# Performance work log

Measured on AMD Instinct MI355X. Metric: run time of the kernel, lower is better.

The kernel has to match this reference:

```python
import jax, jax.numpy as jnp
import numpy as np

N, E = 50000, 800000
IN_CH, HID, OUT = 128, 64, 64
H1, H2 = 4, 1
NEG_SLOPE = 0.2  # PyG GATConv default


def _glorot(key, shape):
    fan_in, fan_out = shape[0], shape[-1]
    lim = (6.0 / (fan_in + fan_out)) ** 0.5
    return jax.random.uniform(key, shape, jnp.float32, -lim, lim)


def setup_inputs() -> dict:
    key = jax.random.key(0)
    ks = jax.random.split(key, 12)
    x = jax.random.normal(ks[0], (N, IN_CH), jnp.float32)
    edge_index = jax.random.randint(ks[1], (2, E), 0, N, jnp.int64)
    # layer 1: in_ch -> hid, 4 heads, concat
    W1 = _glorot(ks[2], (IN_CH, H1 * HID))
    a_src1 = _glorot(ks[3], (H1, HID))
    a_dst1 = _glorot(ks[4], (H1, HID))
    b1 = jnp.zeros((H1 * HID,), jnp.float32)
    # layer 2: hid*4 -> out, 1 head, mean (concat=False)
    W2 = _glorot(ks[5], (H1 * HID, H2 * OUT))
    a_src2 = _glorot(ks[6], (H2, OUT))
    a_dst2 = _glorot(ks[7], (H2, OUT))
    b2 = jnp.zeros((OUT,), jnp.float32)
    return {"x": x, "edge_index": edge_index, "W1": W1, "a_src1": a_src1,
            "a_dst1": a_dst1, "b1": b1, "W2": W2, "a_src2": a_src2,
            "a_dst2": a_dst2, "b2": b2}


def gat_layer(x, src, dst, W, a_src, a_dst, b, concat):
    n = x.shape[0]
    Hh, Fh = a_src.shape
    h = (x @ W).reshape(n, Hh, Fh)                      # [N,H,F]
    al_src = jnp.sum(h * a_src[None], axis=-1)          # [N,H]
    al_dst = jnp.sum(h * a_dst[None], axis=-1)          # [N,H]
    logits = jax.nn.leaky_relu(al_src[src] + al_dst[dst], NEG_SLOPE)  # [E,H]
    # numerically stable segment softmax over destination nodes
    mx = jax.ops.segment_max(logits, dst, num_segments=n)
    mx = jnp.where(jnp.isfinite(mx), mx, 0.0)
    e = jnp.exp(logits - mx[dst])                       # [E,H]
    denom = jax.ops.segment_sum(e, dst, num_segments=n)  # [N,H]
    alpha = e / jnp.maximum(denom[dst], 1e-16)          # [E,H]
    msg = h[src] * alpha[:, :, None]                    # [E,H,F]
    out = jax.ops.segment_sum(msg, dst, num_segments=n)  # [N,H,F]
    out = out.reshape(n, Hh * Fh) if concat else out.mean(axis=1)
    return out + b


def reference(x, edge_index, W1, a_src1, a_dst1, b1, W2, a_src2, a_dst2, b2):
    n = x.shape[0]
    # PyG GATConv adds self-loops by default
    loops = jnp.arange(n, dtype=edge_index.dtype)
    src = jnp.concatenate([edge_index[0], loops])
    dst = jnp.concatenate([edge_index[1], loops])
    h = gat_layer(x, src, dst, W1, a_src1, a_dst1, b1, concat=True)
    h = jax.nn.elu(h)
    # dropout is identity in eval mode
    out = gat_layer(h, src, dst, W2, a_src2, a_dst2, b2, concat=False)
    return out
```

## Files before the change

kernel.cpp:

```cpp
#include <hip/hip_runtime.h>
#include <math.h>

#define NEG_SLOPE 0.2f
#define SLOTS 64

typedef unsigned short ushort_t;
typedef _Float16 f16x8 __attribute__((ext_vector_type(8)));
typedef _Float16 h2v  __attribute__((ext_vector_type(2)));
typedef float f32x4v __attribute__((ext_vector_type(4)));

__device__ __forceinline__ float leaky(float x) { return x > 0.f ? x : NEG_SLOPE * x; }

__device__ __forceinline__ ushort_t f2h(float f) {
    union { _Float16 h; ushort_t u; } v; v.h = (_Float16)f; return v.u;
}
__device__ __forceinline__ unsigned packh(float a, float b) {
    union { h2v h; unsigned u; } c; c.h[0] = (_Float16)a; c.h[1] = (_Float16)b; return c.u;
}

__global__ __launch_bounds__(256) void k_prep0(const float* __restrict__ W1, const float* __restrict__ W2,
                                               const float* __restrict__ as1, const float* __restrict__ ad1,
                                               const float* __restrict__ as2, const float* __restrict__ ad2,
                                               ushort_t* __restrict__ W1t, ushort_t* __restrict__ W2t,
                                               float* __restrict__ va1s, float* __restrict__ va1d,
                                               float* __restrict__ va2s, float* __restrict__ va2d) {
    int b = blockIdx.x, t = threadIdx.x;
    if (b < 256) {
        if (t < 128) W1t[b * 128 + t] = f2h(W1[t * 256 + b]);
    } else if (b < 320) {
        int n = b - 256;
        W2t[n * 256 + t] = f2h(W2[t * 64 + n]);
    } else if (b == 320) {
        for (int idx = t; idx < 1024; idx += 256) {
            int k = idx >> 3, h = (idx >> 1) & 3, sd = idx & 1;
            const float* a = sd ? ad1 : as1;
            float acc = 0.f;
            for (int f = 0; f < 64; ++f) acc += W1[k * 256 + h * 64 + f] * a[h * 64 + f];
            (sd ? va1d : va1s)[k * 4 + h] = acc;
        }
    } else {
        for (int idx = t; idx < 512; idx += 256) {
            int k = idx >> 1, sd = idx & 1;
            const float* a = sd ? ad2 : as2;
            float acc = 0.f;
            for (int f = 0; f < 64; ++f) acc += W2[k * 64 + f] * a[f];
            (sd ? va2d : va2s)[k] = acc;
        }
    }
}

__global__ __launch_bounds__(256) void k_prep1(const int* __restrict__ ei, int E, int EB,
                                               int* __restrict__ cnt, ushort_t* __restrict__ csr,
                                               const float* __restrict__ x,
                                               const float* __restrict__ va1s, const float* __restrict__ va1d,
                                               ushort_t* __restrict__ xh,
                                               float4* __restrict__ alS, float4* __restrict__ alD,
                                               int N, int NB) {
    int b = blockIdx.x, t = threadIdx.x;
    if (b < EB) {
        int i = b * 256 + t;
        if (i < E) {
            int s = ei[i];
            int d = ei[E + i];
            int p = atomicAdd(&cnt[d], 1);
            if (p < SLOTS - 1) csr[d * SLOTS + 1 + p] = (ushort_t)s;
        }
        return;
    }
    b -= EB;
    if (b < NB) {
        int n = b * 256 + t;
        if (n < N) csr[n * SLOTS] = (ushort_t)n;
        return;
    }
    b -= NB;
    int r = b * 16 + (t >> 4);
    int idx = t & 15;
    if (r >= N) return;
    const float* xr = x + (size_t)r * 128 + idx * 8;
    float4 f0 = *(const float4*)xr;
    float4 f1 = *(const float4*)(xr + 4);
    uint4 pv;
    pv.x = packh(f0.x, f0.y); pv.y = packh(f0.z, f0.w);
    pv.z = packh(f1.x, f1.y); pv.w = packh(f1.z, f1.w);
    *(uint4*)&xh[(size_t)r * 128 + idx * 8] = pv;
    float xs[8] = {f0.x, f0.y, f0.z, f0.w, f1.x, f1.y, f1.z, f1.w};
    float s0 = 0, s1 = 0, s2 = 0, s3 = 0, d0 = 0, d1 = 0, d2 = 0, d3 = 0;
    #pragma unroll
    for (int j = 0; j < 8; ++j) {
        int k = idx * 8 + j;
        float4 vs = *(const float4*)&va1s[k * 4];
        float4 vd = *(const float4*)&va1d[k * 4];
        s0 += xs[j] * vs.x; s1 += xs[j] * vs.y; s2 += xs[j] * vs.z; s3 += xs[j] * vs.w;
        d0 += xs[j] * vd.x; d1 += xs[j] * vd.y; d2 += xs[j] * vd.z; d3 += xs[j] * vd.w;
    }
    #pragma unroll
    for (int off = 8; off >= 1; off >>= 1) {
        s0 += __shfl_xor(s0, off, 64); s1 += __shfl_xor(s1, off, 64);
        s2 += __shfl_xor(s2, off, 64); s3 += __shfl_xor(s3, off, 64);
        d0 += __shfl_xor(d0, off, 64); d1 += __shfl_xor(d1, off, 64);
        d2 += __shfl_xor(d2, off, 64); d3 += __shfl_xor(d3, off, 64);
    }
    if (idx == 0) {
        alS[r] = make_float4(s0, s1, s2, s3);
        alD[r] = make_float4(d0, d1, d2, d3);
    }
}

#define CONS(p, a) do { \
    _Float16 ah_ = (_Float16)(a); \
    h2v a2_ = {ah_, ah_}; \
    union { uint4 u; h2v h[4]; } c_; c_.u = (p); \
    ha0 += c_.h[0] * a2_; ha1 += c_.h[1] * a2_; \
    ha2 += c_.h[2] * a2_; ha3 += c_.h[3] * a2_; } while (0)

#define FLUSH() do { \
    acc[0] += (float)ha0[0]; acc[1] += (float)ha0[1]; \
    acc[2] += (float)ha1[0]; acc[3] += (float)ha1[1]; \
    acc[4] += (float)ha2[0]; acc[5] += (float)ha2[1]; \
    acc[6] += (float)ha3[0]; acc[7] += (float)ha3[1]; \
    ha0 = (h2v)0; ha1 = (h2v)0; ha2 = (h2v)0; ha3 = (h2v)0; } while (0)

__global__ __launch_bounds__(256) void k_agg1(const int* __restrict__ cnt, const ushort_t* __restrict__ csr,
                                              const float4* __restrict__ alS4, const float4* __restrict__ alD4,
                                              const ushort_t* __restrict__ xh,
                                              ushort_t* __restrict__ aggh, int N) {
    __shared__ float s_alpha[4][SLOTS][4];
    __shared__ int   s_off[4][SLOTS];
    int w = threadIdx.x >> 6, lane = threadIdx.x & 63;
    int n = blockIdx.x * 4 + w;
    if (n >= N) return;
    int stored = cnt[n]; if (stored > SLOTS - 1) stored = SLOTS - 1;
    int deg = stored + 1;
    int s = 0;
    if (lane < deg) s = csr[(size_t)n * SLOTS + lane];
    s_off[w][lane] = (lane < deg) ? (s << 8) : 0;

    float e0 = 0.f, e1 = 0.f, e2 = 0.f, e3 = 0.f;
    if (lane < deg) {
        float4 ald = alD4[n];
        float4 as = alS4[s];
        e0 = __expf(leaky(as.x + ald.x));
        e1 = __expf(leaky(as.y + ald.y));
        e2 = __expf(leaky(as.z + ald.z));
        e3 = __expf(leaky(as.w + ald.w));
    }
    *(float4*)&s_alpha[w][lane][0] = make_float4(e0, e1, e2, e3);

    int head = lane >> 4, cid = lane & 15;
    const char* xb = (const char*)xh + cid * 16;

    float acc[8];
    #pragma unroll
    for (int i = 0; i < 8; ++i) acc[i] = 0.f;
    h2v ha0 = (h2v)0, ha1 = (h2v)0, ha2 = (h2v)0, ha3 = (h2v)0;

    int nit = (deg + 3) & ~3;

    int4 ovA = *(const int4*)&s_off[w][0];
    uint4 pA0 = *(const uint4*)(xb + ovA.x);
    uint4 pA1 = *(const uint4*)(xb + ovA.y);
    uint4 pA2 = *(const uint4*)(xb + ovA.z);
    uint4 pA3 = *(const uint4*)(xb + ovA.w);

    for (int j = 0; j < nit; j += 8) {
        uint4 pB0, pB1, pB2, pB3;
        bool hasB = (j + 4 < nit);
        if (hasB) {
            int4 ovB = *(const int4*)&s_off[w][j + 4];
            pB0 = *(const uint4*)(xb + ovB.x);
            pB1 = *(const uint4*)(xb + ovB.y);
            pB2 = *(const uint4*)(xb + ovB.z);
            pB3 = *(const uint4*)(xb + ovB.w);
        }
        {
            float a0 = s_alpha[w][j + 0][head];
            float a1 = s_alpha[w][j + 1][head];
            float a2 = s_alpha[w][j + 2][head];
            float a3 = s_alpha[w][j + 3][head];
            CONS(pA0, a0); CONS(pA1, a1); CONS(pA2, a2); CONS(pA3, a3);
        }
        if (hasB) {
            if (j + 8 < nit) {
                int4 ovA2 = *(const int4*)&s_off[w][j + 8];
                pA0 = *(const uint4*)(xb + ovA2.x);
                pA1 = *(const uint4*)(xb + ovA2.y);
                pA2 = *(const uint4*)(xb + ovA2.z);
                pA3 = *(const uint4*)(xb + ovA2.w);
            }
            float a0 = s_alpha[w][j + 4][head];
            float a1 = s_alpha[w][j + 5][head];
            float a2 = s_alpha[w][j + 6][head];
            float a3 = s_alpha[w][j + 7][head];
            CONS(pB0, a0); CONS(pB1, a1); CONS(pB2, a2); CONS(pB3, a3);
        }
        FLUSH();
    }

    float d0 = e0, d1 = e1, d2 = e2, d3 = e3;
    #pragma unroll
    for (int off = 32; off >= 1; off >>= 1) {
        d0 += __shfl_xor(d0, off, 64); d1 += __shfl_xor(d1, off, 64);
        d2 += __shfl_xor(d2, off, 64); d3 += __shfl_xor(d3, off, 64);
    }
    float dh = head == 0 ? d0 : head == 1 ? d1 : head == 2 ? d2 : d3;
    float inv = 1.f / fmaxf(dh, 1e-16f);

    uint4 u;
    u.x = packh(acc[0] * inv, acc[1] * inv);
    u.y = packh(acc[2] * inv, acc[3] * inv);
    u.z = packh(acc[4] * inv, acc[5] * inv);
    u.w = packh(acc[6] * inv, acc[7] * inv);
    *(uint4*)(aggh + (size_t)n * 512 + head * 128 + cid * 8) = u;
}
#undef CONS
#undef FLUSH

__global__ __launch_bounds__(256) void k_gemmO(const ushort_t* __restrict__ aggh, const ushort_t* __restrict__ W1t,
                                               const ushort_t* __restrict__ W2t,
                                               const float* __restrict__ b1,
                                               const float* __restrict__ va2s, const float* __restrict__ va2d,
                                               ushort_t* __restrict__ h2h,
                                               float* __restrict__ al2S, float* __restrict__ al2D, int N) {
    __shared__ ushort_t sU[4 * 64 * 136];
    __shared__ float s_al2w[4][64][2];
    int t = threadIdx.x;
    int w = t >> 6, lane = t & 63;
    int m = lane & 15, quad = lane >> 4;
    int r0 = blockIdx.x * 64;

    #pragma unroll
    for (int q = 0; q < 16; ++q) {
        int idx = t + q * 256;
        int row = idx >> 6, off = idx & 63;
        int gr = r0 + row;
        uint4 v = (gr < N) ? *(const uint4*)(aggh + (size_t)gr * 512 + off * 8)
                           : make_uint4(0, 0, 0, 0);
        int h = off >> 4, k8 = off & 15;
        *(uint4*)&sU[(size_t)(h * 64 + row) * 136 + k8 * 8] = v;
    }
    __syncthreads();

    f32x4v acc[4][4];
    #pragma unroll
    for (int r = 0; r < 4; ++r)
        #pragma unroll
        for (int cg = 0; cg < 4; ++cg) acc[r][cg] = (f32x4v){0.f, 0.f, 0.f, 0.f};
    #pragma unroll
    for (int ks = 0; ks < 4; ++ks) {
        f16x8 af[4];
        #pragma unroll
        for (int r = 0; r < 4; ++r)
            af[r] = *(f16x8*)&sU[(size_t)(w * 64 + r * 16 + m) * 136 + ks * 32 + quad * 8];
        #pragma unroll
        for (int cg = 0; cg < 4; ++cg) {
            f16x8 bf = *(f16x8*)&W1t[(size_t)(w * 64 + cg * 16 + m) * 128 + ks * 32 + quad * 8];
            #pragma unroll
            for (int r = 0; r < 4; ++r)
                acc[r][cg] = __builtin_amdgcn_mfma_f32_16x16x32_f16(af[r], bf, acc[r][cg], 0, 0, 0);
        }
    }
    __syncthreads();

    ushort_t* sO = sU;
    float ps[4][4], pd[4][4];
    #pragma unroll
    for (int r = 0; r < 4; ++r)
        #pragma unroll
        for (int reg = 0; reg < 4; ++reg) { ps[r][reg] = 0.f; pd[r][reg] = 0.f; }
    #pragma unroll
    for (int cg = 0; cg < 4; ++cg) {
        int c = w * 64 + cg * 16 + m;
        float bias = b1[c];
        float v2s = va2s[c], v2d = va2d[c];
        #pragma unroll
        for (int r = 0; r < 4; ++r)
            #pragma unroll
            for (int reg = 0; reg < 4; ++reg) {
                int row = r * 16 + quad * 4 + reg;
                float v = acc[r][cg][reg] + bias;
                v = v > 0.f ? v : (__expf(v) - 1.f);
                sO[(size_t)row * 264 + c] = f2h(v);
                ps[r][reg] += v * v2s;
                pd[r][reg] += v * v2d;
            }
    }
    #pragma unroll
    for (int off = 1; off <= 8; off <<= 1)
        #pragma unroll
        for (int r = 0; r < 4; ++r)
            #pragma unroll
            for (int reg = 0; reg < 4; ++reg) {
                ps[r][reg] += __shfl_xor(ps[r][reg], off, 64);
                pd[r][reg] += __shfl_xor(pd[r][reg], off, 64);
            }
    if (m == 0) {
        #pragma unroll
        for (int r = 0; r < 4; ++r)
            #pragma unroll
            for (int reg = 0; reg < 4; ++reg) {
                int row = r * 16 + quad * 4 + reg;
                s_al2w[w][row][0] = ps[r][reg];
                s_al2w[w][row][1] = pd[r][reg];
            }
    }
    __syncthreads();

    if (t < 64) {
        int gr = r0 + t;
        if (gr < N) {
            float a = 0.f, b = 0.f;
            #pragma unroll
            for (int w2 = 0; w2 < 4; ++w2) { a += s_al2w[w2][t][0]; b += s_al2w[w2][t][1]; }
            al2S[gr] = a; al2D[gr] = b;
        }
    }

    f32x4v acc2[4];
    #pragma unroll
    for (int r = 0; r < 4; ++r) acc2[r] = (f32x4v){0.f, 0.f, 0.f, 0.f};
    #pragma unroll
    for (int kb = 0; kb < 2; ++kb)
        #pragma unroll
        for (int ks = 0; ks < 4; ++ks) {
            int kk = kb * 128 + ks * 32 + quad * 8;
            f16x8 bf = *(f16x8*)&W2t[(size_t)(w * 16 + m) * 256 + kk];
            #pragma unroll
            for (int r = 0; r < 4; ++r) {
                f16x8 af = *(f16x8*)&sO[(size_t)(r * 16 + m) * 264 + kk];
                acc2[r] = __builtin_amdgcn_mfma_f32_16x16x32_f16(af, bf, acc2[r], 0, 0, 0);
            }
        }
    int col = w * 16 + m;
    #pragma unroll
    for (int r = 0; r < 4; ++r) {
        int gr0 = r0 + r * 16 + quad * 4;
        #pragma unroll
        for (int reg = 0; reg < 4; ++reg) {
            int gr = gr0 + reg;
            if (gr < N) h2h[(size_t)gr * 64 + col] = f2h(acc2[r][reg]);
        }
    }
}

__global__ __launch_bounds__(256) void k_agg2(const int* __restrict__ cnt, const ushort_t* __restrict__ csr,
                                              const float* __restrict__ alS, const float* __restrict__ alD,
                                              const ushort_t* __restrict__ h2h, const float* __restrict__ b2,
                                              float* __restrict__ out, int N) {
    int lane = threadIdx.x & 63;
    int n = blockIdx.x * 4 + (threadIdx.x >> 6);
    if (n >= N) return;
    int stored = cnt[n]; if (stored > SLOTS - 1) stored = SLOTS - 1;
    int deg = stored + 1;
    const ushort_t* crow = csr + (size_t)n * SLOTS;

    int s0 = 0;
    if (lane < deg) s0 = crow[lane];

    int grp = lane >> 3, cid = lane & 7;
    int choff = cid * 16;
    const char* hbase = (const char*)h2h;

    uint4 pbuf[3];
    #pragma unroll
    for (int i = 0; i < 3; ++i) {
        int sj = __shfl(s0, i * 8 + grp, 64);
        pbuf[i] = *(const uint4*)(hbase + ((size_t)sj << 7) + choff);
    }

    float ald = alD[n];
    float e0 = 0.f;
    if (lane < deg) e0 = __expf(leaky(alS[s0] + ald));

    h2v ha0 = (h2v)0, ha1 = (h2v)0, ha2 = (h2v)0, ha3 = (h2v)0;
    #pragma unroll
    for (int i = 0; i < 3; ++i) {
        float a = __shfl(e0, i * 8 + grp, 64);
        union { uint4 u; h2v h[4]; } c; c.u = pbuf[i];
        _Float16 ah = (_Float16)a;
        h2v a2 = {ah, ah};
        ha0 += c.h[0] * a2; ha1 += c.h[1] * a2;
        ha2 += c.h[2] * a2; ha3 += c.h[3] * a2;
    }
    for (int j = 24; j < deg; j += 8) {
        int jj = j + grp;
        float a = __shfl(e0, jj, 64);
        int sj = __shfl(s0, jj, 64);
        union { uint4 u; h2v h[4]; } c;
        c.u = *(const uint4*)(hbase + ((size_t)sj << 7) + choff);
        _Float16 ah = (_Float16)a;
        h2v a2 = {ah, ah};
        ha0 += c.h[0] * a2; ha1 += c.h[1] * a2;
        ha2 += c.h[2] * a2; ha3 += c.h[3] * a2;
    }

    float den = e0;
    #pragma unroll
    for (int off = 32; off >= 1; off >>= 1) den += __shfl_xor(den, off, 64);
    float inv = 1.f / fmaxf(den, 1e-16f);

    float acc[8];
    acc[0] = (float)ha0[0]; acc[1] = (float)ha0[1];
    acc[2] = (float)ha1[0]; acc[3] = (float)ha1[1];
    acc[4] = (float)ha2[0]; acc[5] = (float)ha2[1];
    acc[6] = (float)ha3[0]; acc[7] = (float)ha3[1];
    #pragma unroll
    for (int off = 8; off <= 32; off <<= 1)
        #pragma unroll
        for (int i = 0; i < 8; ++i) acc[i] += __shfl_xor(acc[i], off, 64);

    if (grp == 0) {
        int c8 = cid * 8;
        float4 b0 = *(const float4*)&b2[c8];
        float4 b1v = *(const float4*)&b2[c8 + 4];
        float4 o0 = make_float4(acc[0]*inv + b0.x, acc[1]*inv + b0.y, acc[2]*inv + b0.z, acc[3]*inv + b0.w);
        float4 o1 = make_float4(acc[4]*inv + b1v.x, acc[5]*inv + b1v.y, acc[6]*inv + b1v.z, acc[7]*inv + b1v.w);
        *(float4*)(out + (size_t)n * 64 + c8) = o0;
        *(float4*)(out + (size_t)n * 64 + c8 + 4) = o1;
    }
}

extern "C" void kernel_launch(void* const* d_in, const int* in_sizes, int n_in,
                              void* d_out, int out_size, void* d_ws, size_t ws_size,
                              hipStream_t stream) {
    const float* x      = (const float*)d_in[0];
    const int*   ei     = (const int*)d_in[1];
    const float* W1     = (const float*)d_in[2];
    const float* a_src1 = (const float*)d_in[3];
    const float* a_dst1 = (const float*)d_in[4];
    const float* b1     = (const float*)d_in[5];
    const float* W2     = (const float*)d_in[6];
    const float* a_src2 = (const float*)d_in[7];
    const float* a_dst2 = (const float*)d_in[8];
    const float* b2     = (const float*)d_in[9];
    float* out = (float*)d_out;

    int N = in_sizes[0] / 128;
    int E = in_sizes[1] / 2;

    char* ws = (char*)d_ws;
    size_t off = 0;
    auto alloc = [&](size_t bytes) -> void* {
        void* p = ws + off;
        off = (off + bytes + 255) & ~(size_t)255;
        return p;
    };
    ushort_t* xh    = (ushort_t*)alloc((size_t)N * 128 * 2);
    ushort_t* aggh  = (ushort_t*)alloc((size_t)N * 512 * 2);
    ushort_t* h2h   = (ushort_t*)alloc((size_t)N * 64 * 2);
    ushort_t* W1t   = (ushort_t*)alloc(256 * 128 * 2);
    ushort_t* W2t   = (ushort_t*)alloc(64 * 256 * 2);
    float* va1s  = (float*)alloc(128 * 4 * 4);
    float* va1d  = (float*)alloc(128 * 4 * 4);
    float* va2s  = (float*)alloc(256 * 4);
    float* va2d  = (float*)alloc(256 * 4);
    float* alS1  = (float*)alloc((size_t)N * 4 * 4);
    float* alD1  = (float*)alloc((size_t)N * 4 * 4);
    float* alS2  = (float*)alloc((size_t)N * 4);
    float* alD2  = (float*)alloc((size_t)N * 4);
    int*   cnt   = (int*)alloc((size_t)N * 4);
    ushort_t* csr = (ushort_t*)alloc((size_t)N * SLOTS * 2);
    (void)ws_size; (void)n_in; (void)out_size;

    int EB  = (E + 255) / 256;
    int NB  = (N + 255) / 256;
    int XB  = (N + 15) / 16;
    int AB1 = (N + 3) / 4;
    int GO  = (N + 63) / 64;
    int NC4 = (N + 3) / 4;

    hipMemsetAsync(cnt, 0, (size_t)N * 4, stream);

    k_prep0<<<322, 256, 0, stream>>>(W1, W2, a_src1, a_dst1, a_src2, a_dst2,
                                     W1t, W2t, va1s, va1d, va2s, va2d);
    k_prep1<<<EB + NB + XB, 256, 0, stream>>>(ei, E, EB, cnt, csr, x, va1s, va1d,
                                              xh, (float4*)alS1, (float4*)alD1, N, NB);
    k_agg1<<<AB1, 256, 0, stream>>>(cnt, csr,
                                    (const float4*)alS1, (const float4*)alD1,
                                    xh, aggh, N);
    k_gemmO<<<GO, 256, 0, stream>>>(aggh, W1t, W2t, b1, va2s, va2d,
                                    h2h, alS2, alD2, N);
    k_agg2<<<NC4, 256, 0, stream>>>(cnt, csr, alS2, alD2, h2h, b2, out, N);
}
```

Measured before the change: 261.9 us.

## Bucket edge scatter into eight sub-CSRs then merge per node

After: 269.3 us. +2.8%, slower.

```diff
diff --git a/kernel.cpp b/kernel.cpp
--- a/kernel.cpp
+++ b/kernel.cpp
@@ -3,6 +3,7 @@
 
 #define NEG_SLOPE 0.2f
 #define SLOTS 64
+#define XSLOTS 24
 
 typedef unsigned short ushort_t;
 typedef _Float16 f16x8 __attribute__((ext_vector_type(8)));
@@ -50,30 +51,25 @@
 }
 
 __global__ __launch_bounds__(256) void k_prep1(const int* __restrict__ ei, int E, int EB,
-                                               int* __restrict__ cnt, ushort_t* __restrict__ csr,
+                                               int* __restrict__ cnt8, ushort_t* __restrict__ csr8,
                                                const float* __restrict__ x,
                                                const float* __restrict__ va1s, const float* __restrict__ va1d,
                                                ushort_t* __restrict__ xh,
                                                float4* __restrict__ alS, float4* __restrict__ alD,
-                                               int N, int NB) {
+                                               int N) {
     int b = blockIdx.x, t = threadIdx.x;
     if (b < EB) {
         int i = b * 256 + t;
         if (i < E) {
             int s = ei[i];
             int d = ei[E + i];
-            int p = atomicAdd(&cnt[d], 1);
-            if (p < SLOTS - 1) csr[d * SLOTS + 1 + p] = (ushort_t)s;
+            int bkt = b & 7;
+            int p = atomicAdd(&cnt8[bkt * N + d], 1);
+            if (p < XSLOTS) csr8[((size_t)bkt * N + d) * XSLOTS + p] = (ushort_t)s;
         }
         return;
     }
     b -= EB;
-    if (b < NB) {
-        int n = b * 256 + t;
-        if (n < N) csr[n * SLOTS] = (ushort_t)n;
-        return;
-    }
-    b -= NB;
     int r = b * 16 + (t >> 4);
     int idx = t & 15;
     if (r >= N) return;
@@ -105,6 +101,29 @@
         alS[r] = make_float4(s0, s1, s2, s3);
         alD[r] = make_float4(d0, d1, d2, d3);
     }
+}
+
+__global__ __launch_bounds__(256) void k_prep2(const int* __restrict__ cnt8, const ushort_t* __restrict__ csr8,
+                                               int* __restrict__ cnt, ushort_t* __restrict__ csr, int N) {
+    __shared__ ushort_t rows[256][72];
+    int t = threadIdx.x;
+    int n = blockIdx.x * 256 + t;
+    if (n >= N) return;
+    rows[t][0] = (ushort_t)n;
+    int total = 0;
+    #pragma unroll
+    for (int b = 0; b < 8; ++b) {
+        int c = cnt8[b * N + n]; c = c > XSLOTS ? XSLOTS : c;
+        const ushort_t* srcp = csr8 + ((size_t)b * N + n) * XSLOTS;
+        for (int k = 0; k < c; ++k) {
+            if (total < SLOTS - 1) rows[t][1 + total++] = srcp[k];
+        }
+    }
+    cnt[n] = total;
+    uint4* dst = (uint4*)(csr + (size_t)n * SLOTS);
+    const uint4* s4 = (const uint4*)&rows[t][0];
+    #pragma unroll
+    for (int i = 0; i < 8; ++i) dst[i] = s4[i];
 }
 
 #define CONS(p, a) do { \
@@ -460,21 +479,24 @@
     float* alD2  = (float*)alloc((size_t)N * 4);
     int*   cnt   = (int*)alloc((size_t)N * 4);
     ushort_t* csr = (ushort_t*)alloc((size_t)N * SLOTS * 2);
+    int*   cnt8  = (int*)alloc((size_t)N * 8 * 4);
+    ushort_t* csr8 = (ushort_t*)alloc((size_t)N * 8 * XSLOTS * 2);
     (void)ws_size; (void)n_in; (void)out_size;
 
     int EB  = (E + 255) / 256;
-    int NB  = (N + 255) / 256;
     int XB  = (N + 15) / 16;
+    int PB  = (N + 255) / 256;
     int AB1 = (N + 3) / 4;
     int GO  = (N + 63) / 64;
     int NC4 = (N + 3) / 4;
 
-    hipMemsetAsync(cnt, 0, (size_t)N * 4, stream);
+    hipMemsetAsync(cnt8, 0, (size_t)N * 8 * 4, stream);
 
     k_prep0<<<322, 256, 0, stream>>>(W1, W2, a_src1, a_dst1, a_src2, a_dst2,
                                      W1t, W2t, va1s, va1d, va2s, va2d);
-    k_prep1<<<EB + NB + XB, 256, 0, stream>>>(ei, E, EB, cnt, csr, x, va1s, va1d,
-                                              xh, (float4*)alS1, (float4*)alD1, N, NB);
+    k_prep1<<<EB + XB, 256, 0, stream>>>(ei, E, EB, cnt8, csr8, x, va1s, va1d,
+                                         xh, (float4*)alS1, (float4*)alD1, N);
+    k_prep2<<<PB, 256, 0, stream>>>(cnt8, csr8, cnt, csr, N);
     k_agg1<<<AB1, 256, 0, stream>>>(cnt, csr,
                                     (const float4*)alS1, (const float4*)alD1,
                                     xh, aggh, N);
```

## Build CSR via two-level bucket partition instead of global atomics

Applied to the files above, without the earlier changes.

Result: faster. 242.6 us (-7.4%).

```diff
diff --git a/kernel.cpp b/kernel.cpp
--- a/kernel.cpp
+++ b/kernel.cpp
@@ -3,6 +3,7 @@
 
 #define NEG_SLOPE 0.2f
 #define SLOTS 64
+#define PARTB 256
 
 typedef unsigned short ushort_t;
 typedef _Float16 f16x8 __attribute__((ext_vector_type(8)));
@@ -49,31 +50,117 @@
     }
 }
 
-__global__ __launch_bounds__(256) void k_prep1(const int* __restrict__ ei, int E, int EB,
-                                               int* __restrict__ cnt, ushort_t* __restrict__ csr,
-                                               const float* __restrict__ x,
-                                               const float* __restrict__ va1s, const float* __restrict__ va1d,
-                                               ushort_t* __restrict__ xh,
-                                               float4* __restrict__ alS, float4* __restrict__ alD,
-                                               int N, int NB) {
+__global__ __launch_bounds__(256) void k_partA(const int* __restrict__ ei, int E, int CH, int NBKT,
+                                               int* __restrict__ bcnt) {
+    __shared__ int hist[256];
+    int k = blockIdx.x, t = threadIdx.x;
+    hist[t] = 0;
+    __syncthreads();
+    int i0 = k * CH;
+    for (int it = 0; it < CH; it += 256) {
+        int i = i0 + it + t;
+        if (it + t < CH && i < E) {
+            int d = ei[E + i];
+            atomicAdd(&hist[d >> 8], 1);
+        }
+    }
+    __syncthreads();
+    if (t < NBKT) bcnt[t * PARTB + k] = hist[t];
+}
+
+__global__ __launch_bounds__(256) void k_partB1(const int* __restrict__ bcnt,
+                                                int* __restrict__ offs, int* __restrict__ btot) {
+    __shared__ int wsum[4];
+    int t = threadIdx.x, b = blockIdx.x;
+    int c = bcnt[b * PARTB + t];
+    int lane = t & 63, w = t >> 6;
+    int v = c;
+    #pragma unroll
+    for (int off = 1; off < 64; off <<= 1) {
+        int u = __shfl_up(v, off, 64);
+        if (lane >= off) v += u;
+    }
+    if (lane == 63) wsum[w] = v;
+    __syncthreads();
+    int add = 0;
+    for (int ww = 0; ww < w; ++ww) add += wsum[ww];
+    offs[b * PARTB + t] = v - c + add;
+    if (t == 255) btot[b] = v + add;
+}
+
+__global__ __launch_bounds__(256) void k_partB2(const int* __restrict__ btot,
+                                                int* __restrict__ bstart, int NBKT, int E) {
+    __shared__ int wsum[4];
+    int t = threadIdx.x;
+    int c = (t < NBKT) ? btot[t] : 0;
+    int lane = t & 63, w = t >> 6;
+    int v = c;
+    #pragma unroll
+    for (int off = 1; off < 64; off <<= 1) {
+        int u = __shfl_up(v, off, 64);
+        if (lane >= off) v += u;
+    }
+    if (lane == 63) wsum[w] = v;
+    __syncthreads();
+    int add = 0;
+    for (int ww = 0; ww < w; ++ww) add += wsum[ww];
+    if (t < NBKT) bstart[t] = v - c + add;
+    if (t == 0) bstart[NBKT] = E;
+}
+
+__global__ __launch_bounds__(256) void k_partC(const int* __restrict__ ei, int E, int CH, int NBKT,
+                                               const int* __restrict__ offs, const int* __restrict__ bstart,
+                                               unsigned* __restrict__ epk) {
+    __shared__ int cur[256];
+    int k = blockIdx.x, t = threadIdx.x;
+    if (t < NBKT) cur[t] = bstart[t] + offs[t * PARTB + k];
+    __syncthreads();
+    int i0 = k * CH;
+    for (int it = 0; it < CH; it += 256) {
+        int i = i0 + it + t;
+        if (it + t < CH && i < E) {
+            unsigned s = (unsigned)ei[i];
+            unsigned d = (unsigned)ei[E + i];
+            int pos = atomicAdd(&cur[d >> 8], 1);
+            epk[pos] = (d << 16) | s;
+        }
+    }
+}
+
+__global__ __launch_bounds__(256) void k_partD(const unsigned* __restrict__ epk, const int* __restrict__ bstart,
+                                               int* __restrict__ cnt, ushort_t* __restrict__ csr, int N) {
+    __shared__ ushort_t rows[256 * SLOTS];
+    __shared__ int cl[256];
     int b = blockIdx.x, t = threadIdx.x;
-    if (b < EB) {
-        int i = b * 256 + t;
-        if (i < E) {
-            int s = ei[i];
-            int d = ei[E + i];
-            int p = atomicAdd(&cnt[d], 1);
-            if (p < SLOTS - 1) csr[d * SLOTS + 1 + p] = (ushort_t)s;
-        }
-        return;
-    }
-    b -= EB;
-    if (b < NB) {
-        int n = b * 256 + t;
-        if (n < N) csr[n * SLOTS] = (ushort_t)n;
-        return;
-    }
-    b -= NB;
+    for (int i = t; i < 256 * SLOTS / 8; i += 256)
+        *(uint4*)&rows[(size_t)i * 8] = make_uint4(0, 0, 0, 0);
+    cl[t] = 0;
+    __syncthreads();
+    int n0 = b * 256;
+    if (n0 + t < N) rows[t * SLOTS] = (ushort_t)(n0 + t);
+    int e0 = bstart[b], e1 = bstart[b + 1];
+    for (int i = e0 + t; i < e1; i += 256) {
+        unsigned u = epk[i];
+        int dl = (u >> 16) & 255;
+        int slot = atomicAdd(&cl[dl], 1);
+        if (slot < SLOTS - 1) rows[dl * SLOTS + 1 + slot] = (ushort_t)(u & 0xFFFFu);
+    }
+    __syncthreads();
+    int nvalid = N - n0; if (nvalid > 256) nvalid = 256;
+    size_t gbase = (size_t)n0 * SLOTS;
+    for (int i = t; i < nvalid * SLOTS / 8; i += 256)
+        *(uint4*)(csr + gbase + (size_t)i * 8) = *(const uint4*)&rows[(size_t)i * 8];
+    if (t < nvalid) {
+        int c = cl[t]; if (c > SLOTS - 1) c = SLOTS - 1;
+        cnt[n0 + t] = c;
+    }
+}
+
+__global__ __launch_bounds__(256) void k_prep1x(const float* __restrict__ x,
+                                                const float* __restrict__ va1s, const float* __restrict__ va1d,
+                                                ushort_t* __restrict__ xh,
+                                                float4* __restrict__ alS, float4* __restrict__ alD, int N) {
+    int b = blockIdx.x, t = threadIdx.x;
     int r = b * 16 + (t >> 4);
     int idx = t & 15;
     if (r >= N) return;
@@ -460,21 +547,28 @@
     float* alD2  = (float*)alloc((size_t)N * 4);
     int*   cnt   = (int*)alloc((size_t)N * 4);
     ushort_t* csr = (ushort_t*)alloc((size_t)N * SLOTS * 2);
+    int NBKT = (N + 255) >> 8;
+    int*      bcnt  = (int*)alloc((size_t)NBKT * PARTB * 4);
+    int*      offs  = (int*)alloc((size_t)NBKT * PARTB * 4);
+    int*      btot  = (int*)alloc((size_t)NBKT * 4);
+    int*      bstart= (int*)alloc((size_t)(NBKT + 1) * 4);
+    unsigned* epk   = (unsigned*)alloc((size_t)E * 4);
     (void)ws_size; (void)n_in; (void)out_size;
 
-    int EB  = (E + 255) / 256;
-    int NB  = (N + 255) / 256;
+    int CH  = (E + PARTB - 1) / PARTB;
     int XB  = (N + 15) / 16;
     int AB1 = (N + 3) / 4;
     int GO  = (N + 63) / 64;
     int NC4 = (N + 3) / 4;
 
-    hipMemsetAsync(cnt, 0, (size_t)N * 4, stream);
-
     k_prep0<<<322, 256, 0, stream>>>(W1, W2, a_src1, a_dst1, a_src2, a_dst2,
                                      W1t, W2t, va1s, va1d, va2s, va2d);
-    k_prep1<<<EB + NB + XB, 256, 0, stream>>>(ei, E, EB, cnt, csr, x, va1s, va1d,
-                                              xh, (float4*)alS1, (float4*)alD1, N, NB);
+    k_partA<<<PARTB, 256, 0, stream>>>(ei, E, CH, NBKT, bcnt);
+    k_partB1<<<NBKT, 256, 0, stream>>>(bcnt, offs, btot);
+    k_partB2<<<1, 256, 0, stream>>>(btot, bstart, NBKT, E);
+    k_partC<<<PARTB, 256, 0, stream>>>(ei, E, CH, NBKT, offs, bstart, epk);
+    k_partD<<<NBKT, 256, 0, stream>>>(epk, bstart, cnt, csr, N);
+    k_prep1x<<<XB, 256, 0, stream>>>(x, va1s, va1d, xh, (float4*)alS1, (float4*)alD1, N);
     k_agg1<<<AB1, 256, 0, stream>>>(cnt, csr,
                                     (const float4*)alS1, (const float4*)alD1,
                                     xh, aggh, N);
```
